# Optimization experiments

Hardware: AMD Instinct MI355X
Metric: run time of the kernel (lower is better)

## Reference

```python
import jax, jax.numpy as jnp
import numpy as np
from jax import lax

B, C, H, W = 4, 64, 256, 256
T, Q = 16, 0.2
C2 = 2 * C


def conv2d(x, w, b, pad):
    y = lax.conv_general_dilated(x, w, (1, 1), [(pad, pad), (pad, pad)],
                                 dimension_numbers=('NCHW', 'OIHW', 'NCHW'))
    return y + b[None, :, None, None]


def setup_inputs() -> dict:
    key = jax.random.key(0)
    ks = jax.random.split(key, 10)
    x = jax.random.normal(ks[0], (B, C, H, W), dtype=jnp.float32)
    lms = jax.random.normal(ks[1], (B, 4, H, W), dtype=jnp.float32)
    # params (kaiming-ish scale)
    W_conv = jax.random.normal(ks[2], (C2, C, 3, 3), dtype=jnp.float32) * (1.0 / np.sqrt(C * 9))
    b_conv = jnp.zeros((C2,), dtype=jnp.float32)
    W_out = jax.random.normal(ks[3], (4, C2), dtype=jnp.float32) * (1.0 / np.sqrt(C2))  # 1x1 conv as matrix
    b_out = jnp.zeros((4,), dtype=jnp.float32)
    W_aue = jax.random.normal(ks[4], (4, C2, 3, 3), dtype=jnp.float32) * (1.0 / np.sqrt(C2 * 9))
    b_aue = jnp.zeros((4,), dtype=jnp.float32)
    # T Bernoulli(1-q) channel masks, fixed for reproducibility  [T, 2C]
    masks = jax.random.bernoulli(ks[5], 1.0 - Q, (T, C2)).astype(jnp.float32)
    return {"x": x, "lms": lms, "W_conv": W_conv, "b_conv": b_conv,
            "W_out": W_out, "b_out": b_out, "W_aue": W_aue, "b_aue": b_aue,
            "masks": masks}


def reference(x, lms, W_conv, b_conv, W_out, b_out, W_aue, b_aue, masks):
    # feature extraction: 3x3 conv C -> 2C
    h = conv2d(x, W_conv, b_conv, 1)                      # [B, 2C, H, W]
    # MC-dropout samples: out(mask_t * h) == (W_out * mask_t) @ h  (1x1 conv is linear)
    Wt = W_out[None, :, :] * masks[:, None, :]            # [T, 4, 2C]
    samples = jnp.tanh(jnp.einsum('toc,bchw->tbohw', Wt, h)
                       + b_out[None, None, :, None, None]) + lms[None]  # [T, B, 4, H, W]
    mean = jnp.mean(samples, axis=0)
    EU = jnp.var(samples, axis=0, ddof=1)                 # unbiased variance over T
    AU = jax.nn.sigmoid(conv2d(h, W_aue, b_aue, 1))       # [B, 4, H, W]
    return (AU, EU, mean)
```

## Files before the change

kernel.cpp:

```cpp
#include <hip/hip_runtime.h>

#define Bsz 4
#define Cin 64
#define C2c 128
#define Hh 256
#define Ww 256
#define Tt 16
#define HW (Hh*Ww)
#define PLANE (Bsz*4*HW)

typedef __attribute__((ext_vector_type(8))) short bf16x8;
typedef __attribute__((ext_vector_type(4))) float f32x4;

#define XT_OFF  0
#define WBF_OFF 33554432
#define WTB_OFF 33701888
#define AUB_OFF 33718272
#define ZP_OFF  33727488

#define N_WTB 8192
#define N_WBF 73728
#define N_AUB 4608
#define N_ZP  64

__device__ __forceinline__ unsigned short f2bf(float f) {
  union { float f; unsigned u; } cv; cv.f = f;
  unsigned u = cv.u;
  unsigned r = (u + 0x7fffu + ((u >> 16) & 1u)) >> 16;
  return (unsigned short)r;
}

__device__ __forceinline__ unsigned cvtpk(float a, float b) {
  unsigned r;
  asm("v_cvt_pk_bf16_f32 %0, %1, %2" : "=v"(r) : "v"(a), "v"(b));
  return r;
}

union U8 { uint2 u2[2]; uint4 u4; bf16x8 v; };

#define GLOAD16(g, l) __builtin_amdgcn_global_load_lds( \
    (const __attribute__((address_space(1))) unsigned int*)(g), \
    (__attribute__((address_space(3))) unsigned int*)(l), 16, 0, 0)

__global__ __launch_bounds__(256) void xtp_kernel(
    const float* __restrict__ x, const float* __restrict__ W_out,
    const float* __restrict__ masks, const float* __restrict__ Wc,
    const float* __restrict__ W_aue,
    unsigned short* __restrict__ xT, unsigned short* __restrict__ Wtb,
    unsigned short* __restrict__ Wbf, unsigned short* __restrict__ Aub,
    unsigned short* __restrict__ Zp) {
  __shared__ unsigned short xs[64 * 132];
  const int tid = threadIdx.x;

  if (blockIdx.z == 4) {
    int i = (blockIdx.y * 2 + blockIdx.x) * 256 + tid;
    if (i < N_WTB) {
      int to = i >> 7, c = i & 127;
      int t = to >> 2, o = to & 3;
      Wtb[i] = f2bf(W_out[o * C2c + c] * masks[t * C2c + c]);
    } else if (i < N_WTB + N_WBF) {
      int idx = i - N_WTB;
      int j = idx & 7;
      int lane = (idx >> 3) & 63;
      int nt = (idx >> 9) & 7;
      int c = idx >> 12;
      int qq = lane >> 4;
      int tap = c >> 1;
      int ic = (c & 1) * 32 + qq * 8 + j;
      int n = nt * 16 + (lane & 15);
      Wbf[idx] = f2bf(Wc[((size_t)n * Cin + ic) * 9 + tap]);
    } else if (i < N_WTB + N_WBF + N_AUB) {
      int idx = i - N_WTB - N_WBF;
      int m = idx / 1152, k = idx % 1152;
      int tap = k >> 7, c = k & 127;
      Aub[idx] = f2bf(W_aue[((size_t)m * C2c + c) * 9 + tap]);
    } else if (i < N_WTB + N_WBF + N_AUB + N_ZP) {
      Zp[i - N_WTB - N_WBF - N_AUB] = 0;
    }
    return;
  }

  const int x0 = blockIdx.x * 128, y = blockIdx.y, bi = blockIdx.z;
  #pragma unroll
  for (int i = 0; i < 8; ++i) {
    int idx = i * 256 + tid;
    int ic = idx >> 5, xq = idx & 31;
    float4 v = *(const float4*)(x + (((size_t)bi * Cin + ic) * Hh + y) * Ww + x0 + xq * 4);
    *(uint2*)(&xs[ic * 132 + xq * 4]) = make_uint2(cvtpk(v.x, v.y), cvtpk(v.z, v.w));
  }
  __syncthreads();
  #pragma unroll
  for (int j = 0; j < 4; ++j) {
    int idx = j * 256 + tid;
    int px = idx >> 3, icg = idx & 7;
    unsigned short u[8];
    #pragma unroll
    for (int k = 0; k < 8; ++k) u[k] = xs[(icg * 8 + k) * 132 + px];
    *(uint4*)(xT + (((size_t)bi * Hh + y) * Ww + (x0 + px)) * Cin + icg * 8) = *(uint4*)u;
  }
}

__global__ __launch_bounds__(256, 3) void fused_kernel(
    const unsigned short* __restrict__ xT, const unsigned short* __restrict__ Wbf,
    const unsigned short* __restrict__ Wtb, const unsigned short* __restrict__ Aub,
    const unsigned short* __restrict__ Zp,
    const float* __restrict__ bc, const float* __restrict__ b_out,
    const float* __restrict__ b_aue, const float* __restrict__ lms,
    float* __restrict__ out) {
  __shared__ __align__(16) unsigned short sh[23040];
  const int tid = threadIdx.x;
  const int x0 = blockIdx.x * 16, y0 = blockIdx.y * 8, bi = blockIdx.z;

  #pragma unroll
  for (int hf = 0; hf < 2; ++hf) {
    #pragma unroll
    for (int i = 0; i < 4; ++i) {
      int g = i * 256 + tid;
      int r = g >> 2;
      int l = (g & 3) ^ ((r >> 1) & 3);
      int pr = r / 20, pc = r - pr * 20;
      int gy = y0 - 2 + pr, gx = x0 - 2 + pc;
      bool ok = (r < 240) && ((unsigned)gy < Hh) && ((unsigned)gx < Ww);
      const unsigned short* src = ok
        ? xT + (((size_t)bi * Hh + gy) * Ww + gx) * Cin + (hf * 4 + l) * 8
        : Zp;
      GLOAD16(src, &sh[hf * 8192 + g * 8]);
    }
  }

  const int lane = tid & 63, wv = tid >> 6;
  const int n16 = lane & 15, q = lane >> 4;
  const int ph = wv >> 1, oh = wv & 1;

  int rbase[6];
  #pragma unroll
  for (int s = 0; s < 6; ++s) {
    int px = ph * 96 + s * 16 + n16;
    int pr = px / 18, pc = px % 18;
    rbase[s] = pr * 20 + pc;
  }

  f32x4 acc[6][4];
  #pragma unroll
  for (int s = 0; s < 6; ++s)
    #pragma unroll
    for (int mt = 0; mt < 4; ++mt) acc[s][mt] = (f32x4){0.f, 0.f, 0.f, 0.f};

  asm volatile("s_waitcnt vmcnt(4)" ::: "memory");
  __builtin_amdgcn_s_barrier();
  __builtin_amdgcn_sched_barrier(0);

  #pragma unroll
  for (int hf = 0; hf < 2; ++hf) {
    if (hf == 1) {
      asm volatile("s_waitcnt vmcnt(0)" ::: "memory");
      __builtin_amdgcn_s_barrier();
      __builtin_amdgcn_sched_barrier(0);
    }
    #pragma unroll
    for (int tap = 0; tap < 9; ++tap) {
      const int dd = (tap / 3) * 20 + (tap % 3);
      const int c = tap * 2 + hf;
      bf16x8 wfr[4];
      const unsigned short* wb = Wbf + ((size_t)(c * 8 + oh * 4) * 64 + lane) * 8;
      #pragma unroll
      for (int mt = 0; mt < 4; ++mt)
        wfr[mt] = ((const U8*)(wb + mt * 512))->v;
      __builtin_amdgcn_s_setprio(1);
      #pragma unroll
      for (int s = 0; s < 6; ++s) {
        int rr = rbase[s] + dd;
        int a = hf * 8192 + rr * 32 + ((q ^ ((rr >> 1) & 3)) << 3);
        U8 t; t.u4 = *(const uint4*)(&sh[a]);
        #pragma unroll
        for (int mt = 0; mt < 4; ++mt)
          acc[s][mt] =
            __builtin_amdgcn_mfma_f32_16x16x32_bf16(wfr[mt], t.v, acc[s][mt], 0, 0, 0);
      }
      __builtin_amdgcn_s_setprio(0);
    }
  }

  uint2 hp[6][4];
  #pragma unroll
  for (int s = 0; s < 6; ++s) {
    const int px = ph * 96 + s * 16 + n16;
    const int pr = px / 18, pc = px % 18;
    const int gy = y0 - 1 + pr, gx = x0 - 1 + pc;
    const bool valid = ((unsigned)gy < Hh) && ((unsigned)gx < Ww);
    #pragma unroll
    for (int mt = 0; mt < 4; ++mt) {
      const int ocl = oh * 64 + mt * 16 + q * 4;
      const float4 b4 = *(const float4*)(bc + ocl);
      unsigned lo = cvtpk(acc[s][mt][0] + b4.x, acc[s][mt][1] + b4.y);
      unsigned hi = cvtpk(acc[s][mt][2] + b4.z, acc[s][mt][3] + b4.w);
      hp[s][mt] = valid ? make_uint2(lo, hi) : make_uint2(0u, 0u);
    }
  }

  __syncthreads();

  #pragma unroll
  for (int s = 0; s < 6; ++s) {
    const int px = ph * 96 + s * 16 + n16;
    if (px < 180) {
      const int key = px & 15;
      #pragma unroll
      for (int mt = 0; mt < 4; ++mt) {
        const int ocl = oh * 64 + mt * 16 + q * 4;
        int a = px * 128 + (((ocl >> 3) ^ key) << 3) + (q & 1) * 4;
        *(uint2*)(&sh[a]) = hp[s][mt];
      }
    }
  }
  __syncthreads();

  f32x4 accG[2][4];
  f32x4 accA[2];
  #pragma unroll
  for (int nt = 0; nt < 2; ++nt) {
    accA[nt] = (f32x4){0.f, 0.f, 0.f, 0.f};
    #pragma unroll
    for (int mt = 0; mt < 4; ++mt) accG[nt][mt] = (f32x4){0.f, 0.f, 0.f, 0.f};
  }

  #pragma unroll
  for (int kc = 0; kc < 4; ++kc) {
    bf16x8 afr[4];
    #pragma unroll
    for (int mt = 0; mt < 4; ++mt)
      afr[mt] = ((const U8*)(Wtb + (size_t)(mt * 16 + n16) * C2c + kc * 32 + q * 8))->v;
    #pragma unroll
    for (int nt = 0; nt < 2; ++nt) {
      int hr = (wv * 2 + nt + 1) * 18 + n16 + 1;
      int a = hr * 128 + (((kc * 4 + q) ^ (hr & 15)) << 3);
      U8 b; b.u4 = *(const uint4*)(&sh[a]);
      #pragma unroll
      for (int mt = 0; mt < 4; ++mt)
        accG[nt][mt] = __builtin_amdgcn_mfma_f32_16x16x32_bf16(afr[mt], b.v, accG[nt][mt], 0, 0, 0);
    }
  }

  #pragma unroll
  for (int kc = 0; kc < 36; ++kc) {
    const int tap = kc >> 2, co4 = kc & 3;
    const int dy = tap / 3, dx = tap % 3;
    bf16x8 afr = ((const U8*)(Aub + (size_t)(n16 & 3) * 1152 + kc * 32 + q * 8))->v;
    #pragma unroll
    for (int nt = 0; nt < 2; ++nt) {
      int hr = (wv * 2 + nt + dy) * 18 + n16 + dx;
      int a = hr * 128 + (((co4 * 4 + q) ^ (hr & 15)) << 3);
      U8 b; b.u4 = *(const uint4*)(&sh[a]);
      accA[nt] = __builtin_amdgcn_mfma_f32_16x16x32_bf16(afr, b.v, accA[nt], 0, 0, 0);
    }
  }

  const float b0 = b_out[0], b1 = b_out[1], b2 = b_out[2], b3 = b_out[3];
  const float ba = b_aue[q];
  const int px = x0 + n16;
  #pragma unroll
  for (int nt = 0; nt < 2; ++nt) {
    const int y = y0 + wv * 2 + nt;
    float th[4][4];
    #pragma unroll
    for (int mt = 0; mt < 4; ++mt) {
      #pragma unroll
      for (int r = 0; r < 4; ++r) {
        float bo = (r == 0) ? b0 : (r == 1) ? b1 : (r == 2) ? b2 : b3;
        float v = accG[nt][mt][r] + bo;
        float e = __expf(2.f * v);
        th[mt][r] = 1.f - 2.f / (e + 1.f);
      }
    }
    float mean_r[4], eu_r[4];
    #pragma unroll
    for (int r = 0; r < 4; ++r) {
      float s = th[0][r] + th[1][r] + th[2][r] + th[3][r];
      s += __shfl_xor(s, 16);
      s += __shfl_xor(s, 32);
      float m = s * (1.f / 16.f);
      float d0 = th[0][r] - m, d1 = th[1][r] - m, d2 = th[2][r] - m, d3 = th[3][r] - m;
      float vs = d0 * d0 + d1 * d1 + d2 * d2 + d3 * d3;
      vs += __shfl_xor(vs, 16);
      vs += __shfl_xor(vs, 32);
      mean_r[r] = m;
      eu_r[r] = vs * (1.f / 15.f);
    }
    float au_r[4];
    #pragma unroll
    for (int r = 0; r < 4; ++r) au_r[r] = __shfl(accA[nt][r], n16);

    float m_q  = (q == 0) ? mean_r[0] : (q == 1) ? mean_r[1] : (q == 2) ? mean_r[2] : mean_r[3];
    float eu_q = (q == 0) ? eu_r[0]   : (q == 1) ? eu_r[1]   : (q == 2) ? eu_r[2]   : eu_r[3];
    float au_q = (q == 0) ? au_r[0]   : (q == 1) ? au_r[1]   : (q == 2) ? au_r[2]   : au_r[3];
    au_q = 1.f / (1.f + __expf(-(au_q + ba)));
    size_t oidx = ((size_t)(bi * 4 + q)) * HW + (size_t)y * Ww + px;
    float lm = lms[oidx];
    out[oidx] = au_q;
    out[PLANE + oidx] = eu_q;
    out[2 * (size_t)PLANE + oidx] = m_q + lm;
  }
}

extern "C" void kernel_launch(void* const* d_in, const int* in_sizes, int n_in,
                              void* d_out, int out_size, void* d_ws, size_t ws_size,
                              hipStream_t stream) {
  const float* x      = (const float*)d_in[0];
  const float* lms    = (const float*)d_in[1];
  const float* W_conv = (const float*)d_in[2];
  const float* b_conv = (const float*)d_in[3];
  const float* W_out  = (const float*)d_in[4];
  const float* b_out  = (const float*)d_in[5];
  const float* W_aue  = (const float*)d_in[6];
  const float* b_aue  = (const float*)d_in[7];
  const float* masks  = (const float*)d_in[8];
  float* out = (float*)d_out;

  char* ws = (char*)d_ws;
  unsigned short* xT  = (unsigned short*)(ws + XT_OFF);
  unsigned short* Wbf = (unsigned short*)(ws + WBF_OFF);
  unsigned short* Wtb = (unsigned short*)(ws + WTB_OFF);
  unsigned short* Aub = (unsigned short*)(ws + AUB_OFF);
  unsigned short* Zp  = (unsigned short*)(ws + ZP_OFF);

  xtp_kernel<<<dim3(2, 256, 5), dim3(256), 0, stream>>>(x, W_out, masks, W_conv, W_aue,
                                                        xT, Wtb, Wbf, Aub, Zp);
  fused_kernel<<<dim3(16, 32, 4), dim3(256), 0, stream>>>(xT, Wbf, Wtb, Aub, Zp, b_conv,
                                                          b_out, b_aue, lms, out);
}
```

Baseline: 219.5 us.

## Double fused kernel block to 512 threads, halving per-wave pixel work

New measurement: 267.6 us. 1.22x slower.

```diff
diff --git a/kernel.cpp b/kernel.cpp
--- a/kernel.cpp
+++ b/kernel.cpp
@@ -100,7 +100,7 @@
   }
 }
 
-__global__ __launch_bounds__(256, 3) void fused_kernel(
+__global__ __launch_bounds__(512, 4) void fused_kernel(
     const unsigned short* __restrict__ xT, const unsigned short* __restrict__ Wbf,
     const unsigned short* __restrict__ Wtb, const unsigned short* __restrict__ Aub,
     const unsigned short* __restrict__ Zp,
@@ -114,8 +114,8 @@
   #pragma unroll
   for (int hf = 0; hf < 2; ++hf) {
     #pragma unroll
-    for (int i = 0; i < 4; ++i) {
-      int g = i * 256 + tid;
+    for (int i = 0; i < 2; ++i) {
+      int g = i * 512 + tid;
       int r = g >> 2;
       int l = (g & 3) ^ ((r >> 1) & 3);
       int pr = r / 20, pc = r - pr * 20;
@@ -132,21 +132,21 @@
   const int n16 = lane & 15, q = lane >> 4;
   const int ph = wv >> 1, oh = wv & 1;
 
-  int rbase[6];
-  #pragma unroll
-  for (int s = 0; s < 6; ++s) {
-    int px = ph * 96 + s * 16 + n16;
+  int rbase[3];
+  #pragma unroll
+  for (int s = 0; s < 3; ++s) {
+    int px = ph * 48 + s * 16 + n16;
     int pr = px / 18, pc = px % 18;
     rbase[s] = pr * 20 + pc;
   }
 
-  f32x4 acc[6][4];
-  #pragma unroll
-  for (int s = 0; s < 6; ++s)
+  f32x4 acc[3][4];
+  #pragma unroll
+  for (int s = 0; s < 3; ++s)
     #pragma unroll
     for (int mt = 0; mt < 4; ++mt) acc[s][mt] = (f32x4){0.f, 0.f, 0.f, 0.f};
 
-  asm volatile("s_waitcnt vmcnt(4)" ::: "memory");
+  asm volatile("s_waitcnt vmcnt(2)" ::: "memory");
   __builtin_amdgcn_s_barrier();
   __builtin_amdgcn_sched_barrier(0);
 
@@ -168,7 +168,7 @@
         wfr[mt] = ((const U8*)(wb + mt * 512))->v;
       __builtin_amdgcn_s_setprio(1);
       #pragma unroll
-      for (int s = 0; s < 6; ++s) {
+      for (int s = 0; s < 3; ++s) {
         int rr = rbase[s] + dd;
         int a = hf * 8192 + rr * 32 + ((q ^ ((rr >> 1) & 3)) << 3);
         U8 t; t.u4 = *(const uint4*)(&sh[a]);
@@ -181,10 +181,10 @@
     }
   }
 
-  uint2 hp[6][4];
-  #pragma unroll
-  for (int s = 0; s < 6; ++s) {
-    const int px = ph * 96 + s * 16 + n16;
+  uint2 hp[3][4];
+  #pragma unroll
+  for (int s = 0; s < 3; ++s) {
+    const int px = ph * 48 + s * 16 + n16;
     const int pr = px / 18, pc = px % 18;
     const int gy = y0 - 1 + pr, gx = x0 - 1 + pc;
     const bool valid = ((unsigned)gy < Hh) && ((unsigned)gx < Ww);
@@ -201,8 +201,8 @@
   __syncthreads();
 
   #pragma unroll
-  for (int s = 0; s < 6; ++s) {
-    const int px = ph * 96 + s * 16 + n16;
+  for (int s = 0; s < 3; ++s) {
+    const int px = ph * 48 + s * 16 + n16;
     if (px < 180) {
       const int key = px & 15;
       #pragma unroll
@@ -215,14 +215,10 @@
   }
   __syncthreads();
 
-  f32x4 accG[2][4];
-  f32x4 accA[2];
-  #pragma unroll
-  for (int nt = 0; nt < 2; ++nt) {
-    accA[nt] = (f32x4){0.f, 0.f, 0.f, 0.f};
-    #pragma unroll
-    for (int mt = 0; mt < 4; ++mt) accG[nt][mt] = (f32x4){0.f, 0.f, 0.f, 0.f};
-  }
+  f32x4 accG[4];
+  f32x4 accA = (f32x4){0.f, 0.f, 0.f, 0.f};
+  #pragma unroll
+  for (int mt = 0; mt < 4; ++mt) accG[mt] = (f32x4){0.f, 0.f, 0.f, 0.f};
 
   #pragma unroll
   for (int kc = 0; kc < 4; ++kc) {
@@ -230,15 +226,12 @@
     #pragma unroll
     for (int mt = 0; mt < 4; ++mt)
       afr[mt] = ((const U8*)(Wtb + (size_t)(mt * 16 + n16) * C2c + kc * 32 + q * 8))->v;
-    #pragma unroll
-    for (int nt = 0; nt < 2; ++nt) {
-      int hr = (wv * 2 + nt + 1) * 18 + n16 + 1;
-      int a = hr * 128 + (((kc * 4 + q) ^ (hr & 15)) << 3);
-      U8 b; b.u4 = *(const uint4*)(&sh[a]);
-      #pragma unroll
-      for (int mt = 0; mt < 4; ++mt)
-        accG[nt][mt] = __builtin_amdgcn_mfma_f32_16x16x32_bf16(afr[mt], b.v, accG[nt][mt], 0, 0, 0);
-    }
+    int hr = (wv + 1) * 18 + n16 + 1;
+    int a = hr * 128 + (((kc * 4 + q) ^ (hr & 15)) << 3);
+    U8 b; b.u4 = *(const uint4*)(&sh[a]);
+    #pragma unroll
+    for (int mt = 0; mt < 4; ++mt)
+      accG[mt] = __builtin_amdgcn_mfma_f32_16x16x32_bf16(afr[mt], b.v, accG[mt], 0, 0, 0);
   }
 
   #pragma unroll
@@ -246,60 +239,54 @@
     const int tap = kc >> 2, co4 = kc & 3;
     const int dy = tap / 3, dx = tap % 3;
     bf16x8 afr = ((const U8*)(Aub + (size_t)(n16 & 3) * 1152 + kc * 32 + q * 8))->v;
-    #pragma unroll
-    for (int nt = 0; nt < 2; ++nt) {
-      int hr = (wv * 2 + nt + dy) * 18 + n16 + dx;
-      int a = hr * 128 + (((co4 * 4 + q) ^ (hr & 15)) << 3);
-      U8 b; b.u4 = *(const uint4*)(&sh[a]);
-      accA[nt] = __builtin_amdgcn_mfma_f32_16x16x32_bf16(afr, b.v, accA[nt], 0, 0, 0);
-    }
+    int hr = (wv + dy) * 18 + n16 + dx;
+    int a = hr * 128 + (((co4 * 4 + q) ^ (hr & 15)) << 3);
+    U8 b; b.u4 = *(const uint4*)(&sh[a]);
+    accA = __builtin_amdgcn_mfma_f32_16x16x32_bf16(afr, b.v, accA, 0, 0, 0);
   }
 
   const float b0 = b_out[0], b1 = b_out[1], b2 = b_out[2], b3 = b_out[3];
   const float ba = b_aue[q];
   const int px = x0 + n16;
-  #pragma unroll
-  for (int nt = 0; nt < 2; ++nt) {
-    const int y = y0 + wv * 2 + nt;
-    float th[4][4];
-    #pragma unroll
-    for (int mt = 0; mt < 4; ++mt) {
-      #pragma unroll
-      for (int r = 0; r < 4; ++r) {
-        float bo = (r == 0) ? b0 : (r == 1) ? b1 : (r == 2) ? b2 : b3;
-        float v = accG[nt][mt][r] + bo;
-        float e = __expf(2.f * v);
-        th[mt][r] = 1.f - 2.f / (e + 1.f);
-      }
-    }
-    float mean_r[4], eu_r[4];
+  const int y = y0 + wv;
+  float th[4][4];
+  #pragma unroll
+  for (int mt = 0; mt < 4; ++mt) {
     #pragma unroll
     for (int r = 0; r < 4; ++r) {
-      float s = th[0][r] + th[1][r] + th[2][r] + th[3][r];
-      s += __shfl_xor(s, 16);
-      s += __shfl_xor(s, 32);
-      float m = s * (1.f / 16.f);
-      float d0 = th[0][r] - m, d1 = th[1][r] - m, d2 = th[2][r] - m, d3 = th[3][r] - m;
-      float vs = d0 * d0 + d1 * d1 + d2 * d2 + d3 * d3;
-      vs += __shfl_xor(vs, 16);
-      vs += __shfl_xor(vs, 32);
-      mean_r[r] = m;
-      eu_r[r] = vs * (1.f / 15.f);
-    }
-    float au_r[4];
-    #pragma unroll
-    for (int r = 0; r < 4; ++r) au_r[r] = __shfl(accA[nt][r], n16);
-
-    float m_q  = (q == 0) ? mean_r[0] : (q == 1) ? mean_r[1] : (q == 2) ? mean_r[2] : mean_r[3];
-    float eu_q = (q == 0) ? eu_r[0]   : (q == 1) ? eu_r[1]   : (q == 2) ? eu_r[2]   : eu_r[3];
-    float au_q = (q == 0) ? au_r[0]   : (q == 1) ? au_r[1]   : (q == 2) ? au_r[2]   : au_r[3];
-    au_q = 1.f / (1.f + __expf(-(au_q + ba)));
-    size_t oidx = ((size_t)(bi * 4 + q)) * HW + (size_t)y * Ww + px;
-    float lm = lms[oidx];
-    out[oidx] = au_q;
-    out[PLANE + oidx] = eu_q;
-    out[2 * (size_t)PLANE + oidx] = m_q + lm;
-  }
+      float bo = (r == 0) ? b0 : (r == 1) ? b1 : (r == 2) ? b2 : b3;
+      float v = accG[mt][r] + bo;
+      float e = __expf(2.f * v);
+      th[mt][r] = 1.f - 2.f / (e + 1.f);
+    }
+  }
+  float mean_r[4], eu_r[4];
+  #pragma unroll
+  for (int r = 0; r < 4; ++r) {
+    float s = th[0][r] + th[1][r] + th[2][r] + th[3][r];
+    s += __shfl_xor(s, 16);
+    s += __shfl_xor(s, 32);
+    float m = s * (1.f / 16.f);
+    float d0 = th[0][r] - m, d1 = th[1][r] - m, d2 = th[2][r] - m, d3 = th[3][r] - m;
+    float vs = d0 * d0 + d1 * d1 + d2 * d2 + d3 * d3;
+    vs += __shfl_xor(vs, 16);
+    vs += __shfl_xor(vs, 32);
+    mean_r[r] = m;
+    eu_r[r] = vs * (1.f / 15.f);
+  }
+  float au_r[4];
+  #pragma unroll
+  for (int r = 0; r < 4; ++r) au_r[r] = __shfl(accA[r], n16);
+
+  float m_q  = (q == 0) ? mean_r[0] : (q == 1) ? mean_r[1] : (q == 2) ? mean_r[2] : mean_r[3];
+  float eu_q = (q == 0) ? eu_r[0]   : (q == 1) ? eu_r[1]   : (q == 2) ? eu_r[2]   : eu_r[3];
+  float au_q = (q == 0) ? au_r[0]   : (q == 1) ? au_r[1]   : (q == 2) ? au_r[2]   : au_r[3];
+  au_q = 1.f / (1.f + __expf(-(au_q + ba)));
+  size_t oidx = ((size_t)(bi * 4 + q)) * HW + (size_t)y * Ww + px;
+  float lm = lms[oidx];
+  out[oidx] = au_q;
+  out[PLANE + oidx] = eu_q;
+  out[2 * (size_t)PLANE + oidx] = m_q + lm;
 }
 
 extern "C" void kernel_launch(void* const* d_in, const int* in_sizes, int n_in,
@@ -325,6 +312,6 @@
 
   xtp_kernel<<<dim3(2, 256, 5), dim3(256), 0, stream>>>(x, W_out, masks, W_conv, W_aue,
                                                         xT, Wtb, Wbf, Aub, Zp);
-  fused_kernel<<<dim3(16, 32, 4), dim3(256), 0, stream>>>(xT, Wbf, Wtb, Aub, Zp, b_conv,
+  fused_kernel<<<dim3(16, 32, 4), dim3(512), 0, stream>>>(xT, Wbf, Wtb, Aub, Zp, b_conv,
                                                           b_out, b_aue, lms, out);
 }
```

## Stage conv weights through LDS with double-buffered async loads per tap

Applied to the files above, without the earlier changes.

Result: faster. 214.1 us (-2.5%).

```diff
diff --git a/kernel.cpp b/kernel.cpp
--- a/kernel.cpp
+++ b/kernel.cpp
@@ -107,7 +107,7 @@
     const float* __restrict__ bc, const float* __restrict__ b_out,
     const float* __restrict__ b_aue, const float* __restrict__ lms,
     float* __restrict__ out) {
-  __shared__ __align__(16) unsigned short sh[23040];
+  __shared__ __align__(16) unsigned short sh[24576];
   const int tid = threadIdx.x;
   const int x0 = blockIdx.x * 16, y0 = blockIdx.y * 8, bi = blockIdx.z;
 
@@ -127,6 +127,11 @@
       GLOAD16(src, &sh[hf * 8192 + g * 8]);
     }
   }
+  {
+    const unsigned short* wsrc = Wbf;
+    GLOAD16(wsrc + tid * 8, &sh[16384 + tid * 8]);
+    GLOAD16(wsrc + (256 + tid) * 8, &sh[16384 + (256 + tid) * 8]);
+  }
 
   const int lane = tid & 63, wv = tid >> 6;
   const int n16 = lane & 15, q = lane >> 4;
@@ -146,70 +151,68 @@
     #pragma unroll
     for (int mt = 0; mt < 4; ++mt) acc[s][mt] = (f32x4){0.f, 0.f, 0.f, 0.f};
 
-  asm volatile("s_waitcnt vmcnt(4)" ::: "memory");
+  asm volatile("s_waitcnt vmcnt(0)" ::: "memory");
   __builtin_amdgcn_s_barrier();
   __builtin_amdgcn_sched_barrier(0);
 
   #pragma unroll
-  for (int hf = 0; hf < 2; ++hf) {
-    if (hf == 1) {
+  for (int k = 0; k < 18; ++k) {
+    const int hf = (k < 9) ? 0 : 1;
+    const int tap = (k < 9) ? k : k - 9;
+    const int dd = (tap / 3) * 20 + (tap % 3);
+
+    if (k < 17) {
+      const int kn = k + 1;
+      const int cn = (kn < 9) ? 2 * kn : 2 * (kn - 9) + 1;
+      const unsigned short* wsrc = Wbf + (size_t)cn * 4096;
+      unsigned short* wdst = (unsigned short*)&sh[16384 + (kn & 1) * 4096];
+      GLOAD16(wsrc + tid * 8, wdst + tid * 8);
+      GLOAD16(wsrc + (256 + tid) * 8, wdst + (256 + tid) * 8);
+    }
+
+    const int wb_s = 16384 + (k & 1) * 4096;
+    bf16x8 wfr[4];
+    #pragma unroll
+    for (int mt = 0; mt < 4; ++mt)
+      wfr[mt] = ((const U8*)(&sh[wb_s + ((oh * 4 + mt) * 64 + lane) * 8]))->v;
+
+    __builtin_amdgcn_s_setprio(1);
+    #pragma unroll
+    for (int s = 0; s < 6; ++s) {
+      int rr = rbase[s] + dd;
+      int a = hf * 8192 + rr * 32 + ((q ^ ((rr >> 1) & 3)) << 3);
+      U8 t; t.u4 = *(const uint4*)(&sh[a]);
+      #pragma unroll
+      for (int mt = 0; mt < 4; ++mt)
+        acc[s][mt] =
+          __builtin_amdgcn_mfma_f32_16x16x32_bf16(wfr[mt], t.v, acc[s][mt], 0, 0, 0);
+    }
+    __builtin_amdgcn_s_setprio(0);
+
+    if (k < 17) {
       asm volatile("s_waitcnt vmcnt(0)" ::: "memory");
       __builtin_amdgcn_s_barrier();
-      __builtin_amdgcn_sched_barrier(0);
-    }
-    #pragma unroll
-    for (int tap = 0; tap < 9; ++tap) {
-      const int dd = (tap / 3) * 20 + (tap % 3);
-      const int c = tap * 2 + hf;
-      bf16x8 wfr[4];
-      const unsigned short* wb = Wbf + ((size_t)(c * 8 + oh * 4) * 64 + lane) * 8;
-      #pragma unroll
-      for (int mt = 0; mt < 4; ++mt)
-        wfr[mt] = ((const U8*)(wb + mt * 512))->v;
-      __builtin_amdgcn_s_setprio(1);
-      #pragma unroll
-      for (int s = 0; s < 6; ++s) {
-        int rr = rbase[s] + dd;
-        int a = hf * 8192 + rr * 32 + ((q ^ ((rr >> 1) & 3)) << 3);
-        U8 t; t.u4 = *(const uint4*)(&sh[a]);
-        #pragma unroll
-        for (int mt = 0; mt < 4; ++mt)
-          acc[s][mt] =
-            __builtin_amdgcn_mfma_f32_16x16x32_bf16(wfr[mt], t.v, acc[s][mt], 0, 0, 0);
-      }
-      __builtin_amdgcn_s_setprio(0);
-    }
-  }
-
-  uint2 hp[6][4];
-  #pragma unroll
-  for (int s = 0; s < 6; ++s) {
-    const int px = ph * 96 + s * 16 + n16;
-    const int pr = px / 18, pc = px % 18;
-    const int gy = y0 - 1 + pr, gx = x0 - 1 + pc;
-    const bool valid = ((unsigned)gy < Hh) && ((unsigned)gx < Ww);
-    #pragma unroll
-    for (int mt = 0; mt < 4; ++mt) {
-      const int ocl = oh * 64 + mt * 16 + q * 4;
-      const float4 b4 = *(const float4*)(bc + ocl);
-      unsigned lo = cvtpk(acc[s][mt][0] + b4.x, acc[s][mt][1] + b4.y);
-      unsigned hi = cvtpk(acc[s][mt][2] + b4.z, acc[s][mt][3] + b4.w);
-      hp[s][mt] = valid ? make_uint2(lo, hi) : make_uint2(0u, 0u);
-    }
-  }
-
+    }
+  }
   __syncthreads();
 
   #pragma unroll
   for (int s = 0; s < 6; ++s) {
     const int px = ph * 96 + s * 16 + n16;
     if (px < 180) {
+      const int pr = px / 18, pc = px % 18;
+      const int gy = y0 - 1 + pr, gx = x0 - 1 + pc;
+      const bool valid = ((unsigned)gy < Hh) && ((unsigned)gx < Ww);
       const int key = px & 15;
       #pragma unroll
       for (int mt = 0; mt < 4; ++mt) {
         const int ocl = oh * 64 + mt * 16 + q * 4;
+        const float4 b4 = *(const float4*)(bc + ocl);
+        unsigned lo = cvtpk(acc[s][mt][0] + b4.x, acc[s][mt][1] + b4.y);
+        unsigned hi = cvtpk(acc[s][mt][2] + b4.z, acc[s][mt][3] + b4.w);
+        if (!valid) { lo = 0u; hi = 0u; }
         int a = px * 128 + (((ocl >> 3) ^ key) << 3) + (q & 1) * 4;
-        *(uint2*)(&sh[a]) = hp[s][mt];
+        *(uint2*)(&sh[a]) = make_uint2(lo, hi);
       }
     }
   }
```

## Split fused conv kernel into conv1 and post kernels via global hT buffer

Applied to the files above, without the earlier changes.

Measured after the change: 218.8 us. About the same (-0.3%).

```diff
diff --git a/kernel.cpp b/kernel.cpp
--- a/kernel.cpp
+++ b/kernel.cpp
@@ -17,6 +17,8 @@
 #define WTB_OFF 33701888
 #define AUB_OFF 33718272
 #define ZP_OFF  33727488
+#define HT_OFF  33728512ull
+#define WS_NEED (HT_OFF + 67108864ull)
 
 #define N_WTB 8192
 #define N_WBF 73728
@@ -100,6 +102,224 @@
   }
 }
 
+__global__ __launch_bounds__(256, 4) void conv1_kernel(
+    const unsigned short* __restrict__ xT, const unsigned short* __restrict__ Wbf,
+    const unsigned short* __restrict__ Zp, const float* __restrict__ bc,
+    unsigned short* __restrict__ hT) {
+  __shared__ __align__(16) unsigned short sh[16384];
+  const int tid = threadIdx.x;
+  const int x0 = blockIdx.x * 16, y0 = blockIdx.y * 8, bi = blockIdx.z;
+
+  #pragma unroll
+  for (int hf = 0; hf < 2; ++hf) {
+    #pragma unroll
+    for (int i = 0; i < 3; ++i) {
+      int g = i * 256 + tid;
+      int r = g >> 2;
+      int l = (g & 3) ^ ((r >> 1) & 3);
+      int pr = r / 18, pc = r - pr * 18;
+      int gy = y0 - 1 + pr, gx = x0 - 1 + pc;
+      bool ok = (r < 180) && ((unsigned)gy < Hh) && ((unsigned)gx < Ww);
+      const unsigned short* src = ok
+        ? xT + (((size_t)bi * Hh + gy) * Ww + gx) * Cin + (hf * 4 + l) * 8
+        : Zp;
+      GLOAD16(src, &sh[hf * 6144 + g * 8]);
+    }
+  }
+
+  const int lane = tid & 63, wv = tid >> 6;
+  const int n16 = lane & 15, q = lane >> 4;
+  const int ph = wv >> 1, oh = wv & 1;
+
+  int rbase[4];
+  #pragma unroll
+  for (int s = 0; s < 4; ++s) rbase[s] = (ph * 4 + s) * 18 + n16;
+
+  f32x4 acc[4][4];
+  #pragma unroll
+  for (int s = 0; s < 4; ++s)
+    #pragma unroll
+    for (int mt = 0; mt < 4; ++mt) acc[s][mt] = (f32x4){0.f, 0.f, 0.f, 0.f};
+
+  asm volatile("s_waitcnt vmcnt(3)" ::: "memory");
+  __builtin_amdgcn_s_barrier();
+  __builtin_amdgcn_sched_barrier(0);
+
+  #pragma unroll
+  for (int hf = 0; hf < 2; ++hf) {
+    if (hf == 1) {
+      asm volatile("s_waitcnt vmcnt(0)" ::: "memory");
+      __builtin_amdgcn_s_barrier();
+      __builtin_amdgcn_sched_barrier(0);
+    }
+    #pragma unroll
+    for (int tap = 0; tap < 9; ++tap) {
+      const int dd = (tap / 3) * 18 + (tap % 3);
+      const int c = tap * 2 + hf;
+      bf16x8 wfr[4];
+      const unsigned short* wb = Wbf + ((size_t)(c * 8 + oh * 4) * 64 + lane) * 8;
+      #pragma unroll
+      for (int mt = 0; mt < 4; ++mt)
+        wfr[mt] = ((const U8*)(wb + mt * 512))->v;
+      __builtin_amdgcn_s_setprio(1);
+      #pragma unroll
+      for (int s = 0; s < 4; ++s) {
+        int rr = rbase[s] + dd;
+        int a = hf * 6144 + rr * 32 + ((q ^ ((rr >> 1) & 3)) << 3);
+        U8 t; t.u4 = *(const uint4*)(&sh[a]);
+        #pragma unroll
+        for (int mt = 0; mt < 4; ++mt)
+          acc[s][mt] =
+            __builtin_amdgcn_mfma_f32_16x16x32_bf16(wfr[mt], t.v, acc[s][mt], 0, 0, 0);
+      }
+      __builtin_amdgcn_s_setprio(0);
+    }
+  }
+  __syncthreads();
+
+  #pragma unroll
+  for (int s = 0; s < 4; ++s) {
+    const int p = ph * 64 + s * 16 + n16;
+    const int key = p & 15;
+    #pragma unroll
+    for (int mt = 0; mt < 4; ++mt) {
+      const int ocl = oh * 64 + mt * 16 + q * 4;
+      const float4 b4 = *(const float4*)(bc + ocl);
+      unsigned lo = cvtpk(acc[s][mt][0] + b4.x, acc[s][mt][1] + b4.y);
+      unsigned hi = cvtpk(acc[s][mt][2] + b4.z, acc[s][mt][3] + b4.w);
+      int a = p * 128 + (((ocl >> 3) ^ key) << 3) + (q & 1) * 4;
+      *(uint2*)(&sh[a]) = make_uint2(lo, hi);
+    }
+  }
+  __syncthreads();
+
+  #pragma unroll
+  for (int it = 0; it < 8; ++it) {
+    int idx = it * 256 + tid;
+    int rec = idx >> 4, sl = idx & 15;
+    uint4 v = *(const uint4*)(&sh[rec * 128 + ((sl ^ (rec & 15)) << 3)]);
+    int row = rec >> 4, col = rec & 15;
+    size_t gpx = ((size_t)bi * Hh + (y0 + row)) * Ww + (x0 + col);
+    *(uint4*)(hT + gpx * C2c + sl * 8) = v;
+  }
+}
+
+__global__ __launch_bounds__(256, 4) void post_kernel(
+    const unsigned short* __restrict__ hT, const unsigned short* __restrict__ Wtb,
+    const unsigned short* __restrict__ Aub, const unsigned short* __restrict__ Zp,
+    const float* __restrict__ b_out, const float* __restrict__ b_aue,
+    const float* __restrict__ lms, float* __restrict__ out) {
+  __shared__ __align__(16) unsigned short sh[24576];
+  const int tid = threadIdx.x;
+  const int x0 = blockIdx.x * 16, y0 = blockIdx.y * 8, bi = blockIdx.z;
+
+  #pragma unroll
+  for (int i = 0; i < 12; ++i) {
+    int g = i * 256 + tid;
+    int r = g >> 4, sl = g & 15;
+    int l = sl ^ (r & 15);
+    int pr = r / 18, pc = r - pr * 18;
+    int gy = y0 - 1 + pr, gx = x0 - 1 + pc;
+    bool ok = (r < 180) && ((unsigned)gy < Hh) && ((unsigned)gx < Ww);
+    const unsigned short* src = ok
+      ? hT + (((size_t)bi * Hh + gy) * Ww + gx) * C2c + l * 8
+      : Zp;
+    GLOAD16(src, &sh[g * 8]);
+  }
+  asm volatile("s_waitcnt vmcnt(0)" ::: "memory");
+  __builtin_amdgcn_s_barrier();
+  __builtin_amdgcn_sched_barrier(0);
+
+  const int lane = tid & 63, wv = tid >> 6;
+  const int n16 = lane & 15, q = lane >> 4;
+
+  f32x4 accG[2][4];
+  f32x4 accA[2];
+  #pragma unroll
+  for (int nt = 0; nt < 2; ++nt) {
+    accA[nt] = (f32x4){0.f, 0.f, 0.f, 0.f};
+    #pragma unroll
+    for (int mt = 0; mt < 4; ++mt) accG[nt][mt] = (f32x4){0.f, 0.f, 0.f, 0.f};
+  }
+
+  #pragma unroll
+  for (int kc = 0; kc < 4; ++kc) {
+    bf16x8 afr[4];
+    #pragma unroll
+    for (int mt = 0; mt < 4; ++mt)
+      afr[mt] = ((const U8*)(Wtb + (size_t)(mt * 16 + n16) * C2c + kc * 32 + q * 8))->v;
+    #pragma unroll
+    for (int nt = 0; nt < 2; ++nt) {
+      int hr = (wv * 2 + nt + 1) * 18 + n16 + 1;
+      int a = hr * 128 + (((kc * 4 + q) ^ (hr & 15)) << 3);
+      U8 b; b.u4 = *(const uint4*)(&sh[a]);
+      #pragma unroll
+      for (int mt = 0; mt < 4; ++mt)
+        accG[nt][mt] = __builtin_amdgcn_mfma_f32_16x16x32_bf16(afr[mt], b.v, accG[nt][mt], 0, 0, 0);
+    }
+  }
+
+  #pragma unroll
+  for (int kc = 0; kc < 36; ++kc) {
+    const int tap = kc >> 2, co4 = kc & 3;
+    const int dy = tap / 3, dx = tap % 3;
+    bf16x8 afr = ((const U8*)(Aub + (size_t)(n16 & 3) * 1152 + kc * 32 + q * 8))->v;
+    #pragma unroll
+    for (int nt = 0; nt < 2; ++nt) {
+      int hr = (wv * 2 + nt + dy) * 18 + n16 + dx;
+      int a = hr * 128 + (((co4 * 4 + q) ^ (hr & 15)) << 3);
+      U8 b; b.u4 = *(const uint4*)(&sh[a]);
+      accA[nt] = __builtin_amdgcn_mfma_f32_16x16x32_bf16(afr, b.v, accA[nt], 0, 0, 0);
+    }
+  }
+
+  const float b0 = b_out[0], b1 = b_out[1], b2 = b_out[2], b3 = b_out[3];
+  const float ba = b_aue[q];
+  const int px = x0 + n16;
+  #pragma unroll
+  for (int nt = 0; nt < 2; ++nt) {
+    const int y = y0 + wv * 2 + nt;
+    float th[4][4];
+    #pragma unroll
+    for (int mt = 0; mt < 4; ++mt) {
+      #pragma unroll
+      for (int r = 0; r < 4; ++r) {
+        float bo = (r == 0) ? b0 : (r == 1) ? b1 : (r == 2) ? b2 : b3;
+        float v = accG[nt][mt][r] + bo;
+        float e = __expf(2.f * v);
+        th[mt][r] = 1.f - 2.f / (e + 1.f);
+      }
+    }
+    float mean_r[4], eu_r[4];
+    #pragma unroll
+    for (int r = 0; r < 4; ++r) {
+      float s = th[0][r] + th[1][r] + th[2][r] + th[3][r];
+      s += __shfl_xor(s, 16);
+      s += __shfl_xor(s, 32);
+      float m = s * (1.f / 16.f);
+      float d0 = th[0][r] - m, d1 = th[1][r] - m, d2 = th[2][r] - m, d3 = th[3][r] - m;
+      float vs = d0 * d0 + d1 * d1 + d2 * d2 + d3 * d3;
+      vs += __shfl_xor(vs, 16);
+      vs += __shfl_xor(vs, 32);
+      mean_r[r] = m;
+      eu_r[r] = vs * (1.f / 15.f);
+    }
+    float au_r[4];
+    #pragma unroll
+    for (int r = 0; r < 4; ++r) au_r[r] = __shfl(accA[nt][r], n16);
+
+    float m_q  = (q == 0) ? mean_r[0] : (q == 1) ? mean_r[1] : (q == 2) ? mean_r[2] : mean_r[3];
+    float eu_q = (q == 0) ? eu_r[0]   : (q == 1) ? eu_r[1]   : (q == 2) ? eu_r[2]   : eu_r[3];
+    float au_q = (q == 0) ? au_r[0]   : (q == 1) ? au_r[1]   : (q == 2) ? au_r[2]   : au_r[3];
+    au_q = 1.f / (1.f + __expf(-(au_q + ba)));
+    size_t oidx = ((size_t)(bi * 4 + q)) * HW + (size_t)y * Ww + px;
+    float lm = lms[oidx];
+    out[oidx] = au_q;
+    out[PLANE + oidx] = eu_q;
+    out[2 * (size_t)PLANE + oidx] = m_q + lm;
+  }
+}
+
 __global__ __launch_bounds__(256, 3) void fused_kernel(
     const unsigned short* __restrict__ xT, const unsigned short* __restrict__ Wbf,
     const unsigned short* __restrict__ Wtb, const unsigned short* __restrict__ Aub,
@@ -180,36 +400,25 @@
       __builtin_amdgcn_s_setprio(0);
     }
   }
-
-  uint2 hp[6][4];
-  #pragma unroll
-  for (int s = 0; s < 6; ++s) {
-    const int px = ph * 96 + s * 16 + n16;
-    const int pr = px / 18, pc = px % 18;
-    const int gy = y0 - 1 + pr, gx = x0 - 1 + pc;
-    const bool valid = ((unsigned)gy < Hh) && ((unsigned)gx < Ww);
-    #pragma unroll
-    for (int mt = 0; mt < 4; ++mt) {
-      const int ocl = oh * 64 + mt * 16 + q * 4;
-      const float4 b4 = *(const float4*)(bc + ocl);
-      unsigned lo = cvtpk(acc[s][mt][0] + b4.x, acc[s][mt][1] + b4.y);
-      unsigned hi = cvtpk(acc[s][mt][2] + b4.z, acc[s][mt][3] + b4.w);
-      hp[s][mt] = valid ? make_uint2(lo, hi) : make_uint2(0u, 0u);
-    }
-  }
-
   __syncthreads();
 
   #pragma unroll
   for (int s = 0; s < 6; ++s) {
     const int px = ph * 96 + s * 16 + n16;
     if (px < 180) {
+      const int pr = px / 18, pc = px % 18;
+      const int gy = y0 - 1 + pr, gx = x0 - 1 + pc;
+      const bool valid = ((unsigned)gy < Hh) && ((unsigned)gx < Ww);
       const int key = px & 15;
       #pragma unroll
       for (int mt = 0; mt < 4; ++mt) {
         const int ocl = oh * 64 + mt * 16 + q * 4;
+        const float4 b4 = *(const float4*)(bc + ocl);
+        unsigned lo = cvtpk(acc[s][mt][0] + b4.x, acc[s][mt][1] + b4.y);
+        unsigned hi = cvtpk(acc[s][mt][2] + b4.z, acc[s][mt][3] + b4.w);
+        if (!valid) { lo = 0u; hi = 0u; }
         int a = px * 128 + (((ocl >> 3) ^ key) << 3) + (q & 1) * 4;
-        *(uint2*)(&sh[a]) = hp[s][mt];
+        *(uint2*)(&sh[a]) = make_uint2(lo, hi);
       }
     }
   }
@@ -322,9 +531,16 @@
   unsigned short* Wtb = (unsigned short*)(ws + WTB_OFF);
   unsigned short* Aub = (unsigned short*)(ws + AUB_OFF);
   unsigned short* Zp  = (unsigned short*)(ws + ZP_OFF);
+  unsigned short* hT  = (unsigned short*)(ws + HT_OFF);
 
   xtp_kernel<<<dim3(2, 256, 5), dim3(256), 0, stream>>>(x, W_out, masks, W_conv, W_aue,
                                                         xT, Wtb, Wbf, Aub, Zp);
-  fused_kernel<<<dim3(16, 32, 4), dim3(256), 0, stream>>>(xT, Wbf, Wtb, Aub, Zp, b_conv,
-                                                          b_out, b_aue, lms, out);
-}
+  if (ws_size >= WS_NEED) {
+    conv1_kernel<<<dim3(16, 32, 4), dim3(256), 0, stream>>>(xT, Wbf, Zp, b_conv, hT);
+    post_kernel<<<dim3(16, 32, 4), dim3(256), 0, stream>>>(hT, Wtb, Aub, Zp, b_out,
+                                                           b_aue, lms, out);
+  } else {
+    fused_kernel<<<dim3(16, 32, 4), dim3(256), 0, stream>>>(xT, Wbf, Wtb, Aub, Zp, b_conv,
+                                                            b_out, b_aue, lms, out);
+  }
+}
```
